# Kernel tuning notes

Hardware: AMD Instinct MI355X
Metric: run time of the kernel (lower is better)

Reference implementation:

```python
import jax, jax.numpy as jnp
import numpy as np

N_HEADS = 2


def setup_inputs() -> dict:
    key = jax.random.key(0)
    ks = jax.random.split(key, 12)
    B, S, d, g = 4096, 32, 512, 512
    sp = (1.0 / np.sqrt(d))
    sg = (1.0 / np.sqrt(g))
    return {
        "source": jax.random.normal(ks[0], (B, d), jnp.float32),
        "gene": jax.random.normal(ks[1], (B, S, g), jnp.float32),
        "neighbors_padding_mask": jax.random.bernoulli(ks[2], 0.3, (B, S)),
        "mask_n": jax.random.uniform(ks[3], (B, 1), jnp.float32),
        "Wq": jax.random.normal(ks[4], (d, d), jnp.float32) * sp,
        "bq": jax.random.normal(ks[5], (d,), jnp.float32) * 0.02,
        "Wk": jax.random.normal(ks[6], (d, g), jnp.float32) * sg,
        "bk": jax.random.normal(ks[7], (d,), jnp.float32) * 0.02,
        "Wv": jax.random.normal(ks[8], (d, g), jnp.float32) * sg,
        "bv": jax.random.normal(ks[9], (d,), jnp.float32) * 0.02,
        "Wout": jax.random.normal(ks[10], (d, d), jnp.float32) * sp,
        "bout": jax.random.normal(ks[11], (d,), jnp.float32) * 0.02,
    }


def reference(source, gene, neighbors_padding_mask, mask_n,
              Wq, bq, Wk, bk, Wv, bv, Wout, bout):
    # attention_node.forward: 1-query masked MHA over S temporal neighbors.
    B, S, _ = gene.shape
    d = source.shape[1]
    H = N_HEADS
    hd = d // H

    # rows where every neighbor is padded -> unmask slot 0 (torch in-place fix)
    invalid = jnp.all(neighbors_padding_mask, axis=1, keepdims=True)      # [B,1]
    mask = neighbors_padding_mask.at[:, 0].set(
        jnp.where(invalid[:, 0], False, neighbors_padding_mask[:, 0]))

    # separate q/k/v projections (kdim=vdim=n_gene != embed_dim)
    q = (source @ Wq.T + bq) * (hd ** -0.5)                               # [B,d]
    k = gene @ Wk.T + bk                                                  # [B,S,d]
    v = gene @ Wv.T + bv                                                  # [B,S,d]

    qh = q.reshape(B, H, hd)
    kh = k.reshape(B, S, H, hd)
    vh = v.reshape(B, S, H, hd)

    scores = jnp.einsum('bhd,bshd->bhs', qh, kh)                          # [B,H,S]
    scores = jnp.where(mask[:, None, :], -jnp.inf, scores)
    w = jax.nn.softmax(scores, axis=-1)                                   # [B,H,S]

    attn = jnp.einsum('bhs,bshd->bhd', w, vh).reshape(B, d)               # [B,d]
    attn_out = attn @ Wout.T + bout

    # zero rows with no valid neighbors, gate, residual
    attn_out = jnp.where(invalid, jnp.float32(0), attn_out)
    out = attn_out * mask_n + source                                      # [B,d]
    attn_weight = w.mean(axis=1)                                          # avg over heads, [B,S]
    return out, attn_weight
```

## Files before the change

### kernel.cpp

```cpp
#include <hip/hip_runtime.h>
#include <hip/hip_bf16.h>
#include <math.h>
#include <stdint.h>


#define NB 4096
#define SNB 32
#define DM 512

typedef __attribute__((ext_vector_type(8))) short bf16x8;
typedef __attribute__((ext_vector_type(4))) float f32x4;

__device__ __forceinline__ unsigned short f2bf(float f) {
    union { float f; unsigned int u; } v; v.f = f;
    unsigned int u = v.u;
    return (unsigned short)((u + 0x7FFFu + ((u >> 16) & 1u)) >> 16);
}
__device__ __forceinline__ float bf2f(unsigned short s) {
    union { unsigned int u; float f; } v; v.u = ((unsigned int)s) << 16;
    return v.f;
}

__global__ __launch_bounds__(256) void k_prep_cd(
    const float* __restrict__ src, const float* __restrict__ Wq,
    const float* __restrict__ bq, const float* __restrict__ Wk,
    const float* __restrict__ Wv, const float* __restrict__ Wout,
    const float* __restrict__ bv, const float* __restrict__ bout,
    const unsigned int* __restrict__ maskw,
    unsigned short* __restrict__ srcb, float* __restrict__ cb,
    float* __restrict__ e, int* __restrict__ mode,
    unsigned short* __restrict__ C, unsigned short* __restrict__ D)
{
    __shared__ __align__(16) unsigned short As[64 * 40];
    __shared__ __align__(16) unsigned short Bs[64 * 40];
    __shared__ int fF, fH;
    int bid = blockIdx.x, t = threadIdx.x;

    if (bid == 0) {
        if (t == 0) { fF = 0; fH = 0; }
        __syncthreads();
        int lf = 0, lh = 0;
        for (int i = t; i < 32768; i += 256) {
            unsigned int w = maskw[i];
            lf |= (w == 0x3F800000u);
            lh |= ((w & 0xFFFFFF00u) != 0u);
        }
        if (lf) atomicOr(&fF, 1);
        if (lh) atomicOr(&fH, 1);
        __syncthreads();
        if (t == 0) *mode = fF ? 2 : (fH ? 1 : 0);
        return;
    }
    if (bid <= 4) {
        int idx = (bid - 1) * 256 + t;
        int h = idx >> 9, j = idx & 511;
        float a = 0.f;
        for (int i = 0; i < 256; i++)
            a += Wk[(size_t)(h * 256 + i) * 512 + j] * bq[h * 256 + i];
        cb[idx] = 0.0625f * a;
        return;
    }
    if (bid <= 6) {
        int n = (bid - 5) * 256 + t;
        const float4* wr = (const float4*)(Wout + (size_t)n * 512);
        const float4* bv4 = (const float4*)bv;
        float a = bout[n];
        for (int q = 0; q < 128; q++) {
            float4 wv = wr[q], vv = bv4[q];
            a += wv.x * vv.x + wv.y * vv.y + wv.z * vv.z + wv.w * vv.w;
        }
        e[n] = a;
        return;
    }
    if (bid < 263) {
        int base = (bid - 7) * 2048;
        for (int q = 0; q < 8; q++) {
            int idx = base + q * 256 + t;
            float4 v = ((const float4*)src)[idx];
            ushort4 o;
            o.x = f2bf(v.x); o.y = f2bf(v.y); o.z = f2bf(v.z); o.w = f2bf(v.w);
            ((ushort4*)srcb)[idx] = o;
        }
        return;
    }

    int w = t >> 6, l = t & 63;
    int wm = (w >> 1) << 5, wn = (w & 1) << 5;
    int quad = l >> 4, lm = l & 15;
    int sj = t & 63, si8 = (t >> 6) << 3;
    f32x4 acc00 = {0.f,0.f,0.f,0.f}, acc01 = {0.f,0.f,0.f,0.f};
    f32x4 acc10 = {0.f,0.f,0.f,0.f}, acc11 = {0.f,0.f,0.f,0.f};

    unsigned short* outp;
    int ldo;
    if (bid < 391) {
        int tt = bid - 263;
        int j0 = (tt >> 3) << 6, m0 = (tt & 7) << 6;
        int jc = j0 & 511;
        int ib = (j0 >> 9) << 8;
        for (int ic = 0; ic < 8; ic++) {
            int i0 = ib + ic * 32;
            bf16x8 av, bw;
#pragma unroll
            for (int q = 0; q < 8; q++) {
                av[q] = (short)f2bf(Wk[(size_t)(i0 + si8 + q) * 512 + jc + sj] * 0.0625f);
                bw[q] = (short)f2bf(Wq[(size_t)(i0 + si8 + q) * 512 + m0 + sj]);
            }
            *(bf16x8*)(As + sj * 40 + si8) = av;
            *(bf16x8*)(Bs + sj * 40 + si8) = bw;
            __syncthreads();
            bf16x8 a0 = *(const bf16x8*)(As + (wm + lm) * 40 + quad * 8);
            bf16x8 a1 = *(const bf16x8*)(As + (wm + 16 + lm) * 40 + quad * 8);
            bf16x8 b0 = *(const bf16x8*)(Bs + (wn + lm) * 40 + quad * 8);
            bf16x8 b1 = *(const bf16x8*)(Bs + (wn + 16 + lm) * 40 + quad * 8);
            acc00 = __builtin_amdgcn_mfma_f32_16x16x32_bf16(a0, b0, acc00, 0, 0, 0);
            acc01 = __builtin_amdgcn_mfma_f32_16x16x32_bf16(a0, b1, acc01, 0, 0, 0);
            acc10 = __builtin_amdgcn_mfma_f32_16x16x32_bf16(a1, b0, acc10, 0, 0, 0);
            acc11 = __builtin_amdgcn_mfma_f32_16x16x32_bf16(a1, b1, acc11, 0, 0, 0);
            __syncthreads();
        }
        outp = C + (size_t)j0 * 512 + m0; ldo = 512;
    } else {
        int tt = bid - 391;
        int n0 = (tt >> 4) << 6, jh0 = (tt & 15) << 6;
        int jc0 = jh0 & 511;
        int ib = (jh0 >> 9) << 8;
        int ra = t >> 2, ca = (t & 3) << 3;
        for (int ic = 0; ic < 8; ic++) {
            int i0 = ib + ic * 32;
            {
                const float4* p = (const float4*)(Wout + (size_t)(n0 + ra) * 512 + i0 + ca);
                float4 v0 = p[0], v1 = p[1];
                bf16x8 av;
                av[0] = (short)f2bf(v0.x); av[1] = (short)f2bf(v0.y);
                av[2] = (short)f2bf(v0.z); av[3] = (short)f2bf(v0.w);
                av[4] = (short)f2bf(v1.x); av[5] = (short)f2bf(v1.y);
                av[6] = (short)f2bf(v1.z); av[7] = (short)f2bf(v1.w);
                *(bf16x8*)(As + ra * 40 + ca) = av;
            }
            bf16x8 bw;
#pragma unroll
            for (int q = 0; q < 8; q++)
                bw[q] = (short)f2bf(Wv[(size_t)(i0 + si8 + q) * 512 + jc0 + sj]);
            *(bf16x8*)(Bs + sj * 40 + si8) = bw;
            __syncthreads();
            bf16x8 a0 = *(const bf16x8*)(As + (wm + lm) * 40 + quad * 8);
            bf16x8 a1 = *(const bf16x8*)(As + (wm + 16 + lm) * 40 + quad * 8);
            bf16x8 b0 = *(const bf16x8*)(Bs + (wn + lm) * 40 + quad * 8);
            bf16x8 b1 = *(const bf16x8*)(Bs + (wn + 16 + lm) * 40 + quad * 8);
            acc00 = __builtin_amdgcn_mfma_f32_16x16x32_bf16(a0, b0, acc00, 0, 0, 0);
            acc01 = __builtin_amdgcn_mfma_f32_16x16x32_bf16(a0, b1, acc01, 0, 0, 0);
            acc10 = __builtin_amdgcn_mfma_f32_16x16x32_bf16(a1, b0, acc10, 0, 0, 0);
            acc11 = __builtin_amdgcn_mfma_f32_16x16x32_bf16(a1, b1, acc11, 0, 0, 0);
            __syncthreads();
        }
        outp = D + (size_t)n0 * 1024 + jh0; ldo = 1024;
    }
    f32x4 accs[2][2] = {{acc00, acc01}, {acc10, acc11}};
    for (int ms = 0; ms < 2; ms++)
        for (int ns = 0; ns < 2; ns++)
            for (int r = 0; r < 4; r++)
                outp[(size_t)(wm + ms * 16 + quad * 4 + r) * ldo + wn + ns * 16 + lm] =
                    f2bf(accs[ms][ns][r]);
}

template <int EPI>
__global__ __launch_bounds__(256) void k_gemm_bt(
    const unsigned short* __restrict__ A, const unsigned short* __restrict__ Bt,
    void* __restrict__ outp, const float* __restrict__ bias,
    const float* __restrict__ gscale, const float* __restrict__ resid,
    int M, int N, int K)
{
    __shared__ __align__(16) unsigned short As[2][64 * 40];
    __shared__ __align__(16) unsigned short Bs[2][64 * 40];
    int nt = N >> 6;
    int m0 = ((int)blockIdx.x / nt) << 6;
    int n0 = ((int)blockIdx.x % nt) << 6;
    int t = threadIdx.x;
    int w = t >> 6, l = t & 63;
    int wm = (w >> 1) << 5, wn = (w & 1) << 5;
    int quad = l >> 4, lm = l & 15;

    f32x4 acc00 = {0.f,0.f,0.f,0.f}, acc01 = {0.f,0.f,0.f,0.f};
    f32x4 acc10 = {0.f,0.f,0.f,0.f}, acc11 = {0.f,0.f,0.f,0.f};

    int srow = t >> 2, spart = t & 3;
    int chunk = spart >> 1, coff = (spart & 1) << 4;
    const unsigned short* ag = A + (size_t)(m0 + srow) * K + spart * 16;
    const unsigned short* bg = Bt + (size_t)(n0 + srow) * K + spart * 16;
    unsigned short* asl = &As[chunk][srow * 40 + coff];
    unsigned short* bsl = &Bs[chunk][srow * 40 + coff];

    for (int k0 = 0; k0 < K; k0 += 64) {
        *(bf16x8*)asl       = *(const bf16x8*)ag;
        *(bf16x8*)(asl + 8) = *(const bf16x8*)(ag + 8);
        *(bf16x8*)bsl       = *(const bf16x8*)bg;
        *(bf16x8*)(bsl + 8) = *(const bf16x8*)(bg + 8);
        ag += 64; bg += 64;
        __syncthreads();
#pragma unroll
        for (int c = 0; c < 2; c++) {
            bf16x8 a0 = *(const bf16x8*)(&As[c][(wm + lm) * 40 + quad * 8]);
            bf16x8 a1 = *(const bf16x8*)(&As[c][(wm + 16 + lm) * 40 + quad * 8]);
            bf16x8 b0 = *(const bf16x8*)(&Bs[c][(wn + lm) * 40 + quad * 8]);
            bf16x8 b1 = *(const bf16x8*)(&Bs[c][(wn + 16 + lm) * 40 + quad * 8]);
            acc00 = __builtin_amdgcn_mfma_f32_16x16x32_bf16(a0, b0, acc00, 0, 0, 0);
            acc01 = __builtin_amdgcn_mfma_f32_16x16x32_bf16(a0, b1, acc01, 0, 0, 0);
            acc10 = __builtin_amdgcn_mfma_f32_16x16x32_bf16(a1, b0, acc10, 0, 0, 0);
            acc11 = __builtin_amdgcn_mfma_f32_16x16x32_bf16(a1, b1, acc11, 0, 0, 0);
        }
        __syncthreads();
    }
    f32x4 accs[2][2] = {{acc00, acc01}, {acc10, acc11}};
    for (int ms = 0; ms < 2; ms++) {
        for (int ns = 0; ns < 2; ns++) {
            int n = n0 + wn + ns * 16 + lm;
            float bval = bias[n];
            for (int r = 0; r < 4; r++) {
                int m = m0 + wm + ms * 16 + quad * 4 + r;
                float v = accs[ms][ns][r] + bval;
                if (EPI == 0) {
                    ((unsigned short*)outp)[(size_t)m * N + n] = f2bf(v);
                } else {
                    ((float*)outp)[(size_t)m * N + n] =
                        v * gscale[m] + resid[(size_t)m * N + n];
                }
            }
        }
    }
}

__global__ __launch_bounds__(256) void k_attn(
    const float* __restrict__ gene, const unsigned short* __restrict__ QKb,
    const void* __restrict__ maskbuf, const int* __restrict__ modep,
    const float* __restrict__ mask_n,
    unsigned short* __restrict__ G, float* __restrict__ gscale,
    float* __restrict__ aw_out)
{
    __shared__ __align__(16) unsigned short glb[32 * 520];
    __shared__ __align__(16) float sp[4 * 64];
    __shared__ __align__(16) float wls[64];
    __shared__ int msk_s[32];

    int b = blockIdx.x, t = threadIdx.x;
    int w = t >> 6, l = t & 63, quad = l >> 4, lm = l & 15;

    bf16x8 af[4];
    {
        const unsigned short* qp = QKb + (size_t)b * 1024 + (size_t)lm * 512
                                 + w * 128 + quad * 8;
#pragma unroll
        for (int kk = 0; kk < 4; kk++) {
            bf16x8 z = {0,0,0,0,0,0,0,0};
            af[kk] = (lm < 2) ? *(const bf16x8*)(qp + kk * 32) : z;
        }
    }

    const float4* gp = (const float4*)(gene + (size_t)b * (SNB * DM));
    for (int it = 0; it < 8; it++) {
        float4 v0 = gp[t * 2 + it * 512];
        float4 v1 = gp[t * 2 + 1 + it * 512];
        int s = (t >> 6) + it * 4;
        int col = (t & 63) * 8;
        bf16x8 pk;
        pk[0] = (short)f2bf(v0.x); pk[1] = (short)f2bf(v0.y);
        pk[2] = (short)f2bf(v0.z); pk[3] = (short)f2bf(v0.w);
        pk[4] = (short)f2bf(v1.x); pk[5] = (short)f2bf(v1.y);
        pk[6] = (short)f2bf(v1.z); pk[7] = (short)f2bf(v1.w);
        *(bf16x8*)(glb + s * 520 + col) = pk;
    }
    int mode = *modep;
    if (t < 32) {
        size_t moff = (size_t)b * 32 + t;
        int mv;
        if (mode == 1)      mv = ((const unsigned char*)maskbuf)[moff] != 0;
        else if (mode == 2) mv = (((const float*)maskbuf)[moff] != 0.0f);
        else                mv = (((const int*)maskbuf)[moff] != 0);
        msk_s[t] = mv;
    }
    __syncthreads();

    if (t == 0) {
        int all = 1;
        for (int s = 0; s < 32; s++) all &= msk_s[s];
        if (all) msk_s[0] = 0;
        gscale[b] = all ? 0.0f : mask_n[b];
    }

    {
        f32x4 s0 = {0.f,0.f,0.f,0.f}, s1 = {0.f,0.f,0.f,0.f};
        int kb = w * 128;
#pragma unroll
        for (int kk = 0; kk < 4; kk++) {
            int k0 = kb + kk * 32;
            bf16x8 b0 = *(const bf16x8*)(glb + lm * 520 + k0 + quad * 8);
            bf16x8 b1 = *(const bf16x8*)(glb + (16 + lm) * 520 + k0 + quad * 8);
            s0 = __builtin_amdgcn_mfma_f32_16x16x32_bf16(af[kk], b0, s0, 0, 0, 0);
            s1 = __builtin_amdgcn_mfma_f32_16x16x32_bf16(af[kk], b1, s1, 0, 0, 0);
        }
        if (quad == 0) {
            sp[w * 64 + lm] = s0[0];
            sp[w * 64 + 32 + lm] = s0[1];
            sp[w * 64 + 16 + lm] = s1[0];
            sp[w * 64 + 48 + lm] = s1[1];
        }
    }
    __syncthreads();

    if (t < 64) {
        int s = t & 31;
        float v = sp[t] + sp[64 + t] + sp[128 + t] + sp[192 + t];
        int mk = msk_s[s];
        float vm = mk ? -1e30f : v;
        for (int off = 16; off > 0; off >>= 1) vm = fmaxf(vm, __shfl_xor(vm, off, 64));
        float ex = mk ? 0.0f : __expf(v - vm);
        float sm = ex;
        for (int off = 16; off > 0; off >>= 1) sm += __shfl_xor(sm, off, 64);
        wls[t] = ex / sm;
    }
    __syncthreads();

    if (t < 32) aw_out[(size_t)b * 32 + t] = 0.5f * (wls[t] + wls[32 + t]);

    {
        int h = t >> 7, jg = (t & 127) << 2;
        float a0 = 0.f, a1 = 0.f, a2 = 0.f, a3 = 0.f;
        const float* wrow = wls + h * 32;
        for (int s4 = 0; s4 < 8; s4++) {
            float4 wv = *(const float4*)(wrow + s4 * 4);
#pragma unroll
            for (int si = 0; si < 4; si++) {
                int s = s4 * 4 + si;
                ushort4 gv = *(const ushort4*)(glb + s * 520 + jg);
                float wq = (si == 0) ? wv.x : (si == 1) ? wv.y : (si == 2) ? wv.z : wv.w;
                a0 += wq * bf2f(gv.x); a1 += wq * bf2f(gv.y);
                a2 += wq * bf2f(gv.z); a3 += wq * bf2f(gv.w);
            }
        }
        ushort4 ov;
        ov.x = f2bf(a0); ov.y = f2bf(a1); ov.z = f2bf(a2); ov.w = f2bf(a3);
        *(ushort4*)(G + (size_t)b * 1024 + h * 512 + jg) = ov;
    }
}

extern "C" void kernel_launch(void* const* d_in, const int* in_sizes, int n_in,
                              void* d_out, int out_size, void* d_ws, size_t ws_size,
                              hipStream_t stream)
{
    const float* src   = (const float*)d_in[0];
    const float* gene  = (const float*)d_in[1];
    const void*  mask  = d_in[2];
    const float* maskn = (const float*)d_in[3];
    const float* Wq    = (const float*)d_in[4];
    const float* bq    = (const float*)d_in[5];
    const float* Wk    = (const float*)d_in[6];
    const float* Wv    = (const float*)d_in[8];
    const float* bv    = (const float*)d_in[9];
    const float* Wout  = (const float*)d_in[10];
    const float* bout  = (const float*)d_in[11];

    float* out = (float*)d_out;
    float* aw  = out + (size_t)NB * DM;

    char* ws = (char*)d_ws;
    size_t off = 0;
    auto alloc = [&](size_t bytes) -> void* {
        void* p = ws + off;
        off = (off + bytes + 255) & ~((size_t)255);
        return p;
    };
    int* mode            = (int*)alloc(4);
    unsigned short* srcb = (unsigned short*)alloc((size_t)NB * DM * 2);
    unsigned short* Cb   = (unsigned short*)alloc((size_t)1024 * 512 * 2);
    unsigned short* Db   = (unsigned short*)alloc((size_t)512 * 1024 * 2);
    float* cb            = (float*)alloc(1024 * 4);
    float* ev            = (float*)alloc(512 * 4);
    unsigned short* QKb  = (unsigned short*)alloc((size_t)NB * 1024 * 2);
    unsigned short* G    = (unsigned short*)alloc((size_t)NB * 1024 * 2);
    float* gs            = (float*)alloc((size_t)NB * 4);

    k_prep_cd<<<519, 256, 0, stream>>>(src, Wq, bq, Wk, Wv, Wout, bv, bout,
                                       (const unsigned int*)mask,
                                       srcb, cb, ev, mode, Cb, Db);
    k_gemm_bt<0><<<(4096 / 64) * (1024 / 64), 256, 0, stream>>>(
        srcb, Cb, QKb, cb, nullptr, nullptr, 4096, 1024, 512);
    k_attn<<<NB, 256, 0, stream>>>(gene, QKb, mask, mode, maskn, G, gs, aw);
    k_gemm_bt<1><<<(4096 / 64) * (512 / 64), 256, 0, stream>>>(
        G, Db, out, ev, gs, src, 4096, 512, 1024);
}
```

Before: 450.5 us.

## Fuse source bf16 conversion into QK GEMM and compute scores in fp32 during gene load

```diff
diff --git a/kernel.cpp b/kernel.cpp
--- a/kernel.cpp
+++ b/kernel.cpp
@@ -22,12 +22,12 @@
 }
 
 __global__ __launch_bounds__(256) void k_prep_cd(
-    const float* __restrict__ src, const float* __restrict__ Wq,
+    const float* __restrict__ Wq,
     const float* __restrict__ bq, const float* __restrict__ Wk,
     const float* __restrict__ Wv, const float* __restrict__ Wout,
     const float* __restrict__ bv, const float* __restrict__ bout,
     const unsigned int* __restrict__ maskw,
-    unsigned short* __restrict__ srcb, float* __restrict__ cb,
+    float* __restrict__ cb,
     float* __restrict__ e, int* __restrict__ mode,
     unsigned short* __restrict__ C, unsigned short* __restrict__ D)
 {
@@ -72,17 +72,6 @@
         e[n] = a;
         return;
     }
-    if (bid < 263) {
-        int base = (bid - 7) * 2048;
-        for (int q = 0; q < 8; q++) {
-            int idx = base + q * 256 + t;
-            float4 v = ((const float4*)src)[idx];
-            ushort4 o;
-            o.x = f2bf(v.x); o.y = f2bf(v.y); o.z = f2bf(v.z); o.w = f2bf(v.w);
-            ((ushort4*)srcb)[idx] = o;
-        }
-        return;
-    }
 
     int w = t >> 6, l = t & 63;
     int wm = (w >> 1) << 5, wn = (w & 1) << 5;
@@ -93,8 +82,8 @@
 
     unsigned short* outp;
     int ldo;
-    if (bid < 391) {
-        int tt = bid - 263;
+    if (bid < 135) {
+        int tt = bid - 7;
         int j0 = (tt >> 3) << 6, m0 = (tt & 7) << 6;
         int jc = j0 & 511;
         int ib = (j0 >> 9) << 8;
@@ -121,7 +110,7 @@
         }
         outp = C + (size_t)j0 * 512 + m0; ldo = 512;
     } else {
-        int tt = bid - 391;
+        int tt = bid - 135;
         int n0 = (tt >> 4) << 6, jh0 = (tt & 15) << 6;
         int jc0 = jh0 & 511;
         int ib = (jh0 >> 9) << 8;
@@ -164,9 +153,9 @@
                     f2bf(accs[ms][ns][r]);
 }
 
-template <int EPI>
+template <int EPI, int AF32>
 __global__ __launch_bounds__(256) void k_gemm_bt(
-    const unsigned short* __restrict__ A, const unsigned short* __restrict__ Bt,
+    const void* __restrict__ Ap, const unsigned short* __restrict__ Bt,
     void* __restrict__ outp, const float* __restrict__ bias,
     const float* __restrict__ gscale, const float* __restrict__ resid,
     int M, int N, int K)
@@ -186,17 +175,37 @@
 
     int srow = t >> 2, spart = t & 3;
     int chunk = spart >> 1, coff = (spart & 1) << 4;
-    const unsigned short* ag = A + (size_t)(m0 + srow) * K + spart * 16;
+    const unsigned short* ag =
+        (const unsigned short*)Ap + (size_t)(m0 + srow) * K + spart * 16;
+    const float4* agf =
+        (const float4*)((const float*)Ap + (size_t)(m0 + srow) * K) + spart * 4;
     const unsigned short* bg = Bt + (size_t)(n0 + srow) * K + spart * 16;
     unsigned short* asl = &As[chunk][srow * 40 + coff];
     unsigned short* bsl = &Bs[chunk][srow * 40 + coff];
 
     for (int k0 = 0; k0 < K; k0 += 64) {
-        *(bf16x8*)asl       = *(const bf16x8*)ag;
-        *(bf16x8*)(asl + 8) = *(const bf16x8*)(ag + 8);
+        if (AF32) {
+            float4 x0 = agf[0], x1 = agf[1], x2 = agf[2], x3 = agf[3];
+            bf16x8 u0, u1;
+            u0[0] = (short)f2bf(x0.x); u0[1] = (short)f2bf(x0.y);
+            u0[2] = (short)f2bf(x0.z); u0[3] = (short)f2bf(x0.w);
+            u0[4] = (short)f2bf(x1.x); u0[5] = (short)f2bf(x1.y);
+            u0[6] = (short)f2bf(x1.z); u0[7] = (short)f2bf(x1.w);
+            u1[0] = (short)f2bf(x2.x); u1[1] = (short)f2bf(x2.y);
+            u1[2] = (short)f2bf(x2.z); u1[3] = (short)f2bf(x2.w);
+            u1[4] = (short)f2bf(x3.x); u1[5] = (short)f2bf(x3.y);
+            u1[6] = (short)f2bf(x3.z); u1[7] = (short)f2bf(x3.w);
+            *(bf16x8*)asl       = u0;
+            *(bf16x8*)(asl + 8) = u1;
+            agf += 16;
+        } else {
+            *(bf16x8*)asl       = *(const bf16x8*)ag;
+            *(bf16x8*)(asl + 8) = *(const bf16x8*)(ag + 8);
+            ag += 64;
+        }
         *(bf16x8*)bsl       = *(const bf16x8*)bg;
         *(bf16x8*)(bsl + 8) = *(const bf16x8*)(bg + 8);
-        ag += 64; bg += 64;
+        bg += 64;
         __syncthreads();
 #pragma unroll
         for (int c = 0; c < 2; c++) {
@@ -238,85 +247,68 @@
     float* __restrict__ aw_out)
 {
     __shared__ __align__(16) unsigned short glb[32 * 520];
-    __shared__ __align__(16) float sp[4 * 64];
-    __shared__ __align__(16) float wls[64];
-    __shared__ int msk_s[32];
+    __shared__ float sc[64];
+    __shared__ float wls[64];
 
     int b = blockIdx.x, t = threadIdx.x;
-    int w = t >> 6, l = t & 63, quad = l >> 4, lm = l & 15;
-
-    bf16x8 af[4];
+    int w = t >> 6, l = t & 63;
+
+    int mode = *modep;
+    int mk = 0;
+    if (t < 64) {
+        size_t moff = (size_t)b * 32 + (t & 31);
+        if (mode == 1)      mk = ((const unsigned char*)maskbuf)[moff] != 0;
+        else if (mode == 2) mk = (((const float*)maskbuf)[moff] != 0.0f);
+        else                mk = (((const int*)maskbuf)[moff] != 0);
+    }
+
+    float qv0[8], qv1[8];
     {
-        const unsigned short* qp = QKb + (size_t)b * 1024 + (size_t)lm * 512
-                                 + w * 128 + quad * 8;
-#pragma unroll
-        for (int kk = 0; kk < 4; kk++) {
-            bf16x8 z = {0,0,0,0,0,0,0,0};
-            af[kk] = (lm < 2) ? *(const bf16x8*)(qp + kk * 32) : z;
-        }
+        const ushort4* qp = (const ushort4*)(QKb + (size_t)b * 1024) + l * 2;
+        ushort4 a0 = qp[0], a1 = qp[1];
+        ushort4 c0 = qp[128], c1 = qp[129];
+        qv0[0] = bf2f(a0.x); qv0[1] = bf2f(a0.y); qv0[2] = bf2f(a0.z); qv0[3] = bf2f(a0.w);
+        qv0[4] = bf2f(a1.x); qv0[5] = bf2f(a1.y); qv0[6] = bf2f(a1.z); qv0[7] = bf2f(a1.w);
+        qv1[0] = bf2f(c0.x); qv1[1] = bf2f(c0.y); qv1[2] = bf2f(c0.z); qv1[3] = bf2f(c0.w);
+        qv1[4] = bf2f(c1.x); qv1[5] = bf2f(c1.y); qv1[6] = bf2f(c1.z); qv1[7] = bf2f(c1.w);
     }
 
     const float4* gp = (const float4*)(gene + (size_t)b * (SNB * DM));
+#pragma unroll
     for (int it = 0; it < 8; it++) {
         float4 v0 = gp[t * 2 + it * 512];
         float4 v1 = gp[t * 2 + 1 + it * 512];
-        int s = (t >> 6) + it * 4;
-        int col = (t & 63) * 8;
+        int s = w + it * 4;
         bf16x8 pk;
         pk[0] = (short)f2bf(v0.x); pk[1] = (short)f2bf(v0.y);
         pk[2] = (short)f2bf(v0.z); pk[3] = (short)f2bf(v0.w);
         pk[4] = (short)f2bf(v1.x); pk[5] = (short)f2bf(v1.y);
         pk[6] = (short)f2bf(v1.z); pk[7] = (short)f2bf(v1.w);
-        *(bf16x8*)(glb + s * 520 + col) = pk;
-    }
-    int mode = *modep;
-    if (t < 32) {
-        size_t moff = (size_t)b * 32 + t;
-        int mv;
-        if (mode == 1)      mv = ((const unsigned char*)maskbuf)[moff] != 0;
-        else if (mode == 2) mv = (((const float*)maskbuf)[moff] != 0.0f);
-        else                mv = (((const int*)maskbuf)[moff] != 0);
-        msk_s[t] = mv;
+        *(bf16x8*)(glb + s * 520 + l * 8) = pk;
+        float p0 = v0.x * qv0[0] + v0.y * qv0[1] + v0.z * qv0[2] + v0.w * qv0[3]
+                 + v1.x * qv0[4] + v1.y * qv0[5] + v1.z * qv0[6] + v1.w * qv0[7];
+        float p1 = v0.x * qv1[0] + v0.y * qv1[1] + v0.z * qv1[2] + v0.w * qv1[3]
+                 + v1.x * qv1[4] + v1.y * qv1[5] + v1.z * qv1[6] + v1.w * qv1[7];
+        for (int off = 32; off > 0; off >>= 1) {
+            p0 += __shfl_xor(p0, off, 64);
+            p1 += __shfl_xor(p1, off, 64);
+        }
+        if (l == 0) { sc[s] = p0; sc[32 + s] = p1; }
     }
     __syncthreads();
 
-    if (t == 0) {
-        int all = 1;
-        for (int s = 0; s < 32; s++) all &= msk_s[s];
-        if (all) msk_s[0] = 0;
-        gscale[b] = all ? 0.0f : mask_n[b];
-    }
-
-    {
-        f32x4 s0 = {0.f,0.f,0.f,0.f}, s1 = {0.f,0.f,0.f,0.f};
-        int kb = w * 128;
-#pragma unroll
-        for (int kk = 0; kk < 4; kk++) {
-            int k0 = kb + kk * 32;
-            bf16x8 b0 = *(const bf16x8*)(glb + lm * 520 + k0 + quad * 8);
-            bf16x8 b1 = *(const bf16x8*)(glb + (16 + lm) * 520 + k0 + quad * 8);
-            s0 = __builtin_amdgcn_mfma_f32_16x16x32_bf16(af[kk], b0, s0, 0, 0, 0);
-            s1 = __builtin_amdgcn_mfma_f32_16x16x32_bf16(af[kk], b1, s1, 0, 0, 0);
-        }
-        if (quad == 0) {
-            sp[w * 64 + lm] = s0[0];
-            sp[w * 64 + 32 + lm] = s0[1];
-            sp[w * 64 + 16 + lm] = s1[0];
-            sp[w * 64 + 48 + lm] = s1[1];
-        }
-    }
-    __syncthreads();
-
     if (t < 64) {
-        int s = t & 31;
-        float v = sp[t] + sp[64 + t] + sp[128 + t] + sp[192 + t];
-        int mk = msk_s[s];
+        unsigned long long bal = __ballot(mk != 0);
+        int invalid = (bal == 0xFFFFFFFFFFFFFFFFull);
+        if (invalid && (t & 31) == 0) mk = 0;
+        float v = sc[t];
         float vm = mk ? -1e30f : v;
         for (int off = 16; off > 0; off >>= 1) vm = fmaxf(vm, __shfl_xor(vm, off, 64));
         float ex = mk ? 0.0f : __expf(v - vm);
         float sm = ex;
         for (int off = 16; off > 0; off >>= 1) sm += __shfl_xor(sm, off, 64);
         wls[t] = ex / sm;
+        if (t == 0) gscale[b] = invalid ? 0.0f : mask_n[b];
     }
     __syncthreads();
 
@@ -370,7 +362,6 @@
         return p;
     };
     int* mode            = (int*)alloc(4);
-    unsigned short* srcb = (unsigned short*)alloc((size_t)NB * DM * 2);
     unsigned short* Cb   = (unsigned short*)alloc((size_t)1024 * 512 * 2);
     unsigned short* Db   = (unsigned short*)alloc((size_t)512 * 1024 * 2);
     float* cb            = (float*)alloc(1024 * 4);
@@ -379,12 +370,12 @@
     unsigned short* G    = (unsigned short*)alloc((size_t)NB * 1024 * 2);
     float* gs            = (float*)alloc((size_t)NB * 4);
 
-    k_prep_cd<<<519, 256, 0, stream>>>(src, Wq, bq, Wk, Wv, Wout, bv, bout,
+    k_prep_cd<<<263, 256, 0, stream>>>(Wq, bq, Wk, Wv, Wout, bv, bout,
                                        (const unsigned int*)mask,
-                                       srcb, cb, ev, mode, Cb, Db);
-    k_gemm_bt<0><<<(4096 / 64) * (1024 / 64), 256, 0, stream>>>(
-        srcb, Cb, QKb, cb, nullptr, nullptr, 4096, 1024, 512);
+                                       cb, ev, mode, Cb, Db);
+    k_gemm_bt<0, 1><<<(4096 / 64) * (1024 / 64), 256, 0, stream>>>(
+        src, Cb, QKb, cb, nullptr, nullptr, 4096, 1024, 512);
     k_attn<<<NB, 256, 0, stream>>>(gene, QKb, mask, mode, maskn, G, gs, aw);
-    k_gemm_bt<1><<<(4096 / 64) * (512 / 64), 256, 0, stream>>>(
+    k_gemm_bt<1, 0><<<(4096 / 64) * (512 / 64), 256, 0, stream>>>(
         G, Db, out, ev, gs, src, 4096, 512, 1024);
 }
```

New measurement: 458.0 us. Within noise of the previous version (+1.7%).
